# Optimization experiments

Measured on AMD Instinct MI355X. Metric: run time of the kernel, lower is better.

Reference implementation:

```python
import jax, jax.numpy as jnp
import numpy as np

B, SQ, SK, D, H, DFF, L = 8, 1024, 1024, 512, 8, 2048, 2
HD = D // H  # head dim = 64
EPS = 1e-5


def _ln(x, g, b):
    mu = jnp.mean(x, axis=-1, keepdims=True)
    var = jnp.mean((x - mu) ** 2, axis=-1, keepdims=True)
    return (x - mu) * jax.lax.rsqrt(var + EPS) * g + b


def setup_inputs() -> dict:
    key = jax.random.key(0)
    ks = jax.random.split(key, 16)
    std = 0.02
    inp = {
        'q': jax.random.normal(ks[0], (B, SQ, D), jnp.float32),
        'k': jax.random.normal(ks[1], (B, SK, D), jnp.float32),
        'v': jax.random.normal(ks[2], (B, SK, D), jnp.float32),
        # per-layer stacked params (weights stored [in, out])
        'WQ': jax.random.normal(ks[3], (L, D, D), jnp.float32) * std,
        'bQ': jnp.zeros((L, D), jnp.float32),
        'WK': jax.random.normal(ks[4], (L, D, D), jnp.float32) * std,
        'bK': jnp.zeros((L, D), jnp.float32),
        'WV': jax.random.normal(ks[5], (L, D, D), jnp.float32) * std,
        'bV': jnp.zeros((L, D), jnp.float32),
        'WO': jax.random.normal(ks[6], (L, D, D), jnp.float32) * std,
        'bO': jnp.zeros((L, D), jnp.float32),
        'Wf1': jax.random.normal(ks[7], (L, D, DFF), jnp.float32) * std,
        'bf1': jnp.zeros((L, DFF), jnp.float32),
        'Wf2': jax.random.normal(ks[8], (L, DFF, D), jnp.float32) * std,
        'bf2': jnp.zeros((L, D), jnp.float32),
        'ln1_g': jnp.ones((L, D), jnp.float32),
        'ln1_b': jnp.zeros((L, D), jnp.float32),
        'ln2_g': jnp.ones((L, D), jnp.float32),
        'ln2_b': jnp.zeros((L, D), jnp.float32),
        'scale': jnp.full((L,), HD ** -0.5, jnp.float32),       # self.scale init
        'extra_scale': jnp.ones((L,), jnp.float32),             # self.extra_scale init
        'gate_attn': jnp.ones((L,), jnp.float32),
        'gate_ffn': jnp.ones((L,), jnp.float32),
    }
    return inp


def reference(q, k, v, WQ, bQ, WK, bK, WV, bV, WO, bO, Wf1, bf1, Wf2, bf2,
              ln1_g, ln1_b, ln2_g, ln2_b, scale, extra_scale, gate_attn, gate_ffn):
    prev = None  # Realformer residual attention scores
    for i in range(L):
        # QKV projections -> [B, H, S, HD]
        qh = (jnp.einsum('bsd,de->bse', q, WQ[i]) + bQ[i]).reshape(B, SQ, H, HD).transpose(0, 2, 1, 3)
        kh = (jnp.einsum('bsd,de->bse', k, WK[i]) + bK[i]).reshape(B, SK, H, HD).transpose(0, 2, 1, 3)
        vh = (jnp.einsum('bsd,de->bse', v, WV[i]) + bV[i]).reshape(B, SK, H, HD).transpose(0, 2, 1, 3)
        eff_scale = scale[i] * jnp.clip(extra_scale[i], 0.01, 50.0)
        scores = jnp.einsum('bhqd,bhkd->bhqk', qh, kh) * eff_scale  # [B,H,SQ,SK]
        if prev is not None:
            scores = scores + prev
        attn = jax.nn.softmax(scores, axis=-1)
        out = jnp.einsum('bhqk,bhkd->bhqd', attn, vh)
        out = out.transpose(0, 2, 1, 3).reshape(B, SQ, D)
        out = jnp.einsum('bsd,de->bse', out, WO[i]) + bO[i]
        # gated residual + post-norm
        q = q + jax.nn.softplus(gate_attn[i]) * out
        q = _ln(q, ln1_g[i], ln1_b[i])
        # FFN (exact gelu like torch default)
        ff = jax.nn.gelu(jnp.einsum('bsd,df->bsf', q, Wf1[i]) + bf1[i], approximate=False)
        ff = jnp.einsum('bsf,fd->bsd', ff, Wf2[i]) + bf2[i]
        q = q + jax.nn.softplus(gate_ffn[i]) * ff
        q = _ln(q, ln2_g[i], ln2_b[i])
        prev = scores
    return q
```

## Files before the change

### kernel.cpp

```cpp
#include <hip/hip_runtime.h>

#define B_   8
#define SQ_  1024
#define SK_  1024
#define D_   512
#define H_   8
#define DFF_ 2048
#define L_   2
#define HD_  64
#define M_   8192

typedef __bf16 bf16;
using bf16x8 = __attribute__((ext_vector_type(8))) __bf16;
using f32x4  = __attribute__((ext_vector_type(4))) float;

__device__ inline f32x4 mfma16(bf16x8 a, bf16x8 b, f32x4 c) {
  return __builtin_amdgcn_mfma_f32_16x16x32_bf16(a, b, c, 0, 0, 0);
}

__device__ __forceinline__ void gl2lds16(const bf16* g, bf16* l) {
  __builtin_amdgcn_global_load_lds(
      (const __attribute__((address_space(1))) void*)g,
      (__attribute__((address_space(3))) void*)l, 16, 0, 0);
}

__device__ __forceinline__ float gelu_fast(float x) {
  float u = 1.5957691216f * (x + 0.044715f * x * x * x);
  return x / (1.0f + __expf(-u));
}

struct TP4 { const float* in[4]; bf16* out[4]; };
__global__ __launch_bounds__(256) void transpose4_k(TP4 p) {
  __shared__ bf16 tile[32][33];
  int z = blockIdx.z, wsel = z >> 1, l = z & 1;
  const float* inp  = p.in[wsel]  + (size_t)l * D_ * D_;
  bf16*        outp = p.out[wsel] + (size_t)l * D_ * D_;
  int c0 = blockIdx.x * 32, r0 = blockIdx.y * 32;
  int tx = threadIdx.x & 31, ty = threadIdx.x >> 5;
#pragma unroll
  for (int i = 0; i < 32; i += 8)
    tile[ty + i][tx] = (bf16)inp[(size_t)(r0 + ty + i) * D_ + c0 + tx];
  __syncthreads();
#pragma unroll
  for (int i = 0; i < 32; i += 8)
    outp[(size_t)(c0 + ty + i) * D_ + r0 + tx] = tile[tx][ty + i];
}

__global__ __launch_bounds__(256) void transpose_k(
    const float* __restrict__ in, bf16* __restrict__ out, int R, int C) {
  __shared__ bf16 tile[32][33];
  const float* inp  = in  + (size_t)blockIdx.z * R * C;
  bf16*        outp = out + (size_t)blockIdx.z * R * C;
  int c0 = blockIdx.x * 32, r0 = blockIdx.y * 32;
  int tx = threadIdx.x & 31, ty = threadIdx.x >> 5;
#pragma unroll
  for (int i = 0; i < 32; i += 8)
    tile[ty + i][tx] = (bf16)inp[(size_t)(r0 + ty + i) * C + c0 + tx];
  __syncthreads();
#pragma unroll
  for (int i = 0; i < 32; i += 8)
    outp[(size_t)(c0 + ty + i) * R + r0 + tx] = tile[tx][ty + i];
}

__global__ __launch_bounds__(256) void f2b3_k(
    const float* __restrict__ a, const float* __restrict__ b,
    const float* __restrict__ c, bf16* __restrict__ oa,
    bf16* __restrict__ ob, bf16* __restrict__ oc) {
  int which = blockIdx.y;
  const float* in = (which == 0) ? a : (which == 1) ? b : c;
  bf16* out = (which == 0) ? oa : (which == 1) ? ob : oc;
  int i = (blockIdx.x * 256 + threadIdx.x) * 4;
  float4 v = *(const float4*)&in[i];
  out[i] = (bf16)v.x; out[i + 1] = (bf16)v.y;
  out[i + 2] = (bf16)v.z; out[i + 3] = (bf16)v.w;
}

template<int BN>
__global__ __launch_bounds__(256) void gemm_t(
    const bf16* __restrict__ A, const bf16* __restrict__ Bt,
    const float* __restrict__ bias, bf16* __restrict__ Cb,
    float* __restrict__ Cf, int Nsz, int Ksz, int gelu) {
  constexpr int NI = BN / 32;
  __shared__ bf16 As[2][128 * 32];
  __shared__ bf16 Bs[2][BN * 32];
  const int tid = threadIdx.x;
  const int m0 = blockIdx.x * 128, n0 = blockIdx.y * BN;
  const int w = tid >> 6, lane = tid & 63, quad = lane >> 4, l16 = lane & 15;
  const int wm = (w & 1) << 6, wn = (w >> 1) * (BN / 2);
  const int r4 = lane >> 2;
  const int k8 = (lane & 3) * 8;
  f32x4 acc[4][NI] = {};

  auto stage = [&](int k0, int buf) {
    gl2lds16(&A[(size_t)(m0 + w * 16 + r4) * Ksz + k0 + k8],
             &As[buf][(w * 16) * 32]);
    gl2lds16(&A[(size_t)(m0 + (w + 4) * 16 + r4) * Ksz + k0 + k8],
             &As[buf][((w + 4) * 16) * 32]);
    gl2lds16(&Bt[(size_t)(n0 + w * 16 + r4) * Ksz + k0 + k8],
             &Bs[buf][(w * 16) * 32]);
    if constexpr (BN == 128)
      gl2lds16(&Bt[(size_t)(n0 + (w + 4) * 16 + r4) * Ksz + k0 + k8],
               &Bs[buf][((w + 4) * 16) * 32]);
  };

  stage(0, 0);
  __syncthreads();
  int buf = 0;
  for (int k0 = 0; k0 < Ksz; k0 += 32, buf ^= 1) {
    if (k0 + 32 < Ksz) stage(k0 + 32, buf ^ 1);
    bf16x8 af[4], bfr[NI];
#pragma unroll
    for (int i = 0; i < 4; i++)
      af[i] = *(const bf16x8*)&As[buf][(wm + i * 16 + l16) * 32 + quad * 8];
#pragma unroll
    for (int i = 0; i < NI; i++)
      bfr[i] = *(const bf16x8*)&Bs[buf][(wn + i * 16 + l16) * 32 + quad * 8];
#pragma unroll
    for (int mi = 0; mi < 4; mi++)
#pragma unroll
      for (int ni = 0; ni < NI; ni++)
        acc[mi][ni] = mfma16(af[mi], bfr[ni], acc[mi][ni]);
    __syncthreads();
  }
#pragma unroll
  for (int mi = 0; mi < 4; mi++)
#pragma unroll
    for (int ni = 0; ni < NI; ni++) {
      int col = n0 + wn + ni * 16 + l16;
      float bv = bias[col];
#pragma unroll
      for (int r = 0; r < 4; r++) {
        int row = m0 + wm + mi * 16 + quad * 4 + r;
        float x = acc[mi][ni][r] + bv;
        if (gelu) x = gelu_fast(x);
        size_t idx = (size_t)row * Nsz + col;
        if (Cb) Cb[idx] = (bf16)x;
        if (Cf) Cf[idx] = x;
      }
    }
}

struct G256 { const bf16* A; const bf16* Bt; const float* bias; bf16* C; };

#define MFB(mh) \
  _Pragma("unroll") \
  for (int mi = 0; mi < 4; mi++) { \
    _Pragma("unroll") \
    for (int ni = 0; ni < 4; ni++) \
      acc[(mh) * 4 + mi][ni] = mfma16(a[mi], b[ni], acc[(mh) * 4 + mi][ni]); \
  }

#define PHASE(s, mh, STAGE, VM) \
  { \
    if ((mh) == 0) { \
      a[0] = ldA(s, 0); a[1] = ldA(s, 1); a[2] = ldA(s, 2); a[3] = ldA(s, 3); \
      b[0] = ldB(s, 0); b[1] = ldB(s, 1); b[2] = ldB(s, 2); b[3] = ldB(s, 3); \
    } else { \
      a[0] = ldA(s, 4); a[1] = ldA(s, 5); a[2] = ldA(s, 6); a[3] = ldA(s, 7); \
    } \
    STAGE; \
    VM; \
    __builtin_amdgcn_s_barrier(); \
    asm volatile("s_waitcnt lgkmcnt(0)" ::: "memory"); \
    __builtin_amdgcn_sched_barrier(0); \
    __builtin_amdgcn_s_setprio(1); \
    MFB(mh); \
    __builtin_amdgcn_s_setprio(0); \
    __builtin_amdgcn_s_barrier(); \
  }

__global__ __launch_bounds__(512, 2) void gemm256_k(G256 g0, G256 g1,
                                                    int Nsz, int Ksz,
                                                    int gelu) {
  __shared__ bf16 As[4 * 8192];
  __shared__ bf16 Bs[4 * 8192];
  const G256 g = blockIdx.z ? g1 : g0;
  const int tid = threadIdx.x;
  const int w = tid >> 6, lane = tid & 63;
  const int quad = lane >> 4, l16 = lane & 15;
  const int wm = w >> 2, wn = w & 3;
  const int m0 = blockIdx.x * 256, n0 = blockIdx.y * 256;
  const int NCH = Ksz >> 5;
  const int ITERS = NCH >> 2;

  const int srow = tid >> 2;
  const int ssw = ((tid & 3) ^ (srow & 3) ^ ((srow >> 2) & 3)) << 3;
  const int swr = ((quad ^ (l16 & 3) ^ (l16 >> 2)) << 3);

  auto stageA = [&](int kc, int s) {
    const bf16* gp = g.A + (size_t)(m0 + srow) * Ksz + kc * 32 + ssw;
    gl2lds16(gp, &As[s * 8192 + w * 512]);
    gl2lds16(gp + (size_t)128 * Ksz, &As[s * 8192 + 4096 + w * 512]);
  };
  auto stageB = [&](int kc, int s) {
    const bf16* gp = g.Bt + (size_t)(n0 + srow) * Ksz + kc * 32 + ssw;
    gl2lds16(gp, &Bs[s * 8192 + w * 512]);
    gl2lds16(gp + (size_t)128 * Ksz, &Bs[s * 8192 + 4096 + w * 512]);
  };
  auto ldA = [&](int s, int mi) {
    return *(const bf16x8*)&As[s * 8192 + (wm * 128 + mi * 16 + l16) * 32 + swr];
  };
  auto ldB = [&](int s, int ni) {
    return *(const bf16x8*)&Bs[s * 8192 + (wn * 64 + ni * 16 + l16) * 32 + swr];
  };

  f32x4 acc[8][4] = {};

  stageA(0, 0); stageB(0, 0);
  stageA(1, 1); stageB(1, 1);
  stageA(2, 2); stageB(2, 2);
  asm volatile("s_waitcnt vmcnt(4)" ::: "memory");
  __builtin_amdgcn_s_barrier();

  for (int it = 0; it < ITERS; ++it) {
    const int c = it * 4;
    const bool last = (it + 1 == ITERS);
    bf16x8 a[4], b[4];
    PHASE(0, 0, stageA(c + 3, 3), )
    PHASE(0, 1, stageB(c + 3, 3), )
    PHASE(1, 0, if (!last) stageA(c + 4, 0), )
    PHASE(1, 1, if (!last) stageB(c + 4, 0),
          if (!last) { asm volatile("s_waitcnt vmcnt(4)" ::: "memory"); }
          else { asm volatile("s_waitcnt vmcnt(0)" ::: "memory"); })
    PHASE(2, 0, if (!last) stageA(c + 5, 1), )
    PHASE(2, 1, if (!last) stageB(c + 5, 1), )
    PHASE(3, 0, if (!last) stageA(c + 6, 2), )
    PHASE(3, 1, if (!last) stageB(c + 6, 2),
          asm volatile("s_waitcnt vmcnt(4)" ::: "memory"))
  }

#pragma unroll
  for (int mi = 0; mi < 8; mi++)
#pragma unroll
    for (int ni = 0; ni < 4; ni++) {
      const int col = n0 + wn * 64 + ni * 16 + l16;
      const float bv = g.bias[col];
#pragma unroll
      for (int r = 0; r < 4; r++) {
        const int row = m0 + wm * 128 + mi * 16 + quad * 4 + r;
        float x = acc[mi][ni][r] + bv;
        if (gelu) x = gelu_fast(x);
        g.C[(size_t)row * Nsz + col] = (bf16)x;
      }
    }
}

__global__ __launch_bounds__(256) void vtrans2_k(const bf16* __restrict__ vhh,
                                                 bf16* __restrict__ vt0,
                                                 bf16* __restrict__ vt1) {
  __shared__ bf16 sm[64][72];
  int kt = blockIdx.x, bh = blockIdx.y, z = blockIdx.z;
  int coloff = z ? D_ : 0;
  bf16* vt = z ? vt1 : vt0;
  int b = bh >> 3, h = bh & 7;
  int tid = threadIdx.x;
  for (int c = tid; c < 512; c += 256) {
    int key = c >> 3, off = (c & 7) * 8;
    *(uint4*)&sm[key][off] = *(const uint4*)
        &vhh[(size_t)(b * SK_ + kt * 64 + key) * (2 * D_) + coloff + h * 64 + off];
  }
  __syncthreads();
  for (int c = tid; c < 512; c += 256) {
    int hd = c >> 3, koff = (c & 7) * 8;
    bf16 tmp[8];
#pragma unroll
    for (int j = 0; j < 8; j++) tmp[j] = sm[koff + j][hd];
    *(uint4*)&vt[(size_t)(bh * 64 + hd) * SK_ + kt * 64 + koff] = *(uint4*)tmp;
  }
}

template<bool HAS0>
__global__ __launch_bounds__(256) void attn_t(
    const bf16* __restrict__ qh, const bf16* __restrict__ qh0,
    const bf16* __restrict__ kh, const bf16* __restrict__ kh0, int kstride,
    const bf16* __restrict__ vt, const float* __restrict__ scale,
    const float* __restrict__ extra, int li, bf16* __restrict__ ctx) {
  __shared__ bf16 Ks[2 * 2 * 2048];
  __shared__ bf16 K0s[HAS0 ? 2 * 2 * 2048 : 64];
  __shared__ bf16 Vs[2 * 2 * 2048];
  __shared__ bf16 Ps[4][16 * 72];
  int qt = blockIdx.x, bh = blockIdx.y;
  int b = bh >> 3, h = bh & 7;
  int tid = threadIdx.x, w = tid >> 6, lane = tid & 63;
  int quad = lane >> 4, l16 = lane & 15;
  const int r4 = lane >> 2, c4 = (lane & 3) * 8;
  float eff1 = scale[li] * fminf(fmaxf(extra[li], 0.01f), 50.0f);
  float eff0 = HAS0 ? scale[li - 1] * fminf(fmaxf(extra[li - 1], 0.01f), 50.0f) : 0.f;
  bf16x8 aq[2][2], aq0[2][2];
#pragma unroll
  for (int mi = 0; mi < 2; mi++) {
    int qrow = b * SQ_ + qt * 128 + w * 32 + mi * 16 + l16;
    const bf16* qp = qh + (size_t)qrow * D_ + h * 64 + quad * 8;
    aq[mi][0] = *(const bf16x8*)qp; aq[mi][1] = *(const bf16x8*)(qp + 32);
#pragma unroll
    for (int k2 = 0; k2 < 2; k2++)
#pragma unroll
      for (int j = 0; j < 8; j++)
        aq[mi][k2][j] = (bf16)((float)aq[mi][k2][j] * eff1);
    if constexpr (HAS0) {
      const bf16* qp0 = qh0 + (size_t)qrow * D_ + h * 64 + quad * 8;
      aq0[mi][0] = *(const bf16x8*)qp0; aq0[mi][1] = *(const bf16x8*)(qp0 + 32);
#pragma unroll
      for (int k2 = 0; k2 < 2; k2++)
#pragma unroll
        for (int j = 0; j < 8; j++)
          aq0[mi][k2][j] = (bf16)((float)aq0[mi][k2][j] * eff0);
    }
  }
  bf16x8 ones;
#pragma unroll
  for (int j = 0; j < 8; j++) ones[j] = (bf16)1.0f;

  f32x4 o[2][4] = {};
  f32x4 ol[2] = {};

  auto stage = [&](int kt, int bufi) {
    size_t kg = (size_t)(b * SK_ + kt * 64 + w * 16 + r4) * kstride + h * 64 + c4;
    gl2lds16(&kh[kg],      &Ks[(bufi * 2 + 0) * 2048 + (w * 16) * 32]);
    gl2lds16(&kh[kg + 32], &Ks[(bufi * 2 + 1) * 2048 + (w * 16) * 32]);
    if constexpr (HAS0) {
      gl2lds16(&kh0[kg],      &K0s[(bufi * 2 + 0) * 2048 + (w * 16) * 32]);
      gl2lds16(&kh0[kg + 32], &K0s[(bufi * 2 + 1) * 2048 + (w * 16) * 32]);
    }
    size_t vg = (size_t)(bh * 64 + w * 16 + r4) * SK_ + kt * 64 + c4;
    gl2lds16(&vt[vg],      &Vs[(bufi * 2 + 0) * 2048 + (w * 16) * 32]);
    gl2lds16(&vt[vg + 32], &Vs[(bufi * 2 + 1) * 2048 + (w * 16) * 32]);
  };

  stage(0, 0);
  __syncthreads();
  int buf = 0;
  for (int kt = 0; kt < SK_ / 64; kt++, buf ^= 1) {
    if (kt + 1 < SK_ / 64) stage(kt + 1, buf ^ 1);
    bf16x8 bv[2][4];
#pragma unroll
    for (int kk = 0; kk < 2; kk++)
#pragma unroll
      for (int ni = 0; ni < 4; ni++)
        bv[kk][ni] = *(const bf16x8*)&Vs[kk * 2048 + buf * 4096 +
                                         (ni * 16 + l16) * 32 + quad * 8];
#pragma unroll
    for (int mi = 0; mi < 2; mi++) {
#pragma unroll
      for (int ni = 0; ni < 4; ni++) {
        int ro = (ni * 16 + l16) * 32 + quad * 8;
        f32x4 t = {};
        t = mfma16(aq[mi][0], *(const bf16x8*)&Ks[0 * 2048 + buf * 4096 + ro], t);
        t = mfma16(aq[mi][1], *(const bf16x8*)&Ks[1 * 2048 + buf * 4096 + ro], t);
        if constexpr (HAS0) {
          t = mfma16(aq0[mi][0], *(const bf16x8*)&K0s[0 * 2048 + buf * 4096 + ro], t);
          t = mfma16(aq0[mi][1], *(const bf16x8*)&K0s[1 * 2048 + buf * 4096 + ro], t);
        }
#pragma unroll
        for (int r = 0; r < 4; r++)
          Ps[w][(quad * 4 + r) * 72 + ni * 16 + l16] = (bf16)__expf(t[r]);
      }
#pragma unroll
      for (int kk = 0; kk < 2; kk++) {
        bf16x8 ap = *(const bf16x8*)&Ps[w][l16 * 72 + kk * 32 + quad * 8];
        ol[mi] = mfma16(ap, ones, ol[mi]);
#pragma unroll
        for (int ni = 0; ni < 4; ni++)
          o[mi][ni] = mfma16(ap, bv[kk][ni], o[mi][ni]);
      }
    }
    __syncthreads();
  }
#pragma unroll
  for (int mi = 0; mi < 2; mi++)
#pragma unroll
    for (int ni = 0; ni < 4; ni++)
#pragma unroll
      for (int r = 0; r < 4; r++) {
        int row = b * SQ_ + qt * 128 + w * 32 + mi * 16 + quad * 4 + r;
        ctx[(size_t)row * D_ + h * 64 + ni * 16 + l16] =
            (bf16)(o[mi][ni][r] / ol[mi][r]);
      }
}

__global__ __launch_bounds__(256) void ln_k(
    const float* __restrict__ cur_in, const float* __restrict__ add,
    const float* __restrict__ gate, const float* __restrict__ g,
    const float* __restrict__ bb, float* __restrict__ outf,
    bf16* __restrict__ outb) {
  int row = blockIdx.x, tid = threadIdx.x;
  float gv = gate[0];
  float sp = gv > 20.f ? gv : log1pf(expf(gv));
  size_t base = (size_t)row * D_;
  int c0 = tid * 2;
  float2 c2 = *(const float2*)&cur_in[base + c0];
  float2 a2 = *(const float2*)&add[base + c0];
  float x0 = c2.x + sp * a2.x, x1 = c2.y + sp * a2.y;
  float s = x0 + x1, s2 = x0 * x0 + x1 * x1;
#pragma unroll
  for (int m = 1; m < 64; m <<= 1) {
    s += __shfl_xor(s, m);
    s2 += __shfl_xor(s2, m);
  }
  __shared__ float sa[4], sb[4];
  int w = tid >> 6;
  if ((tid & 63) == 0) { sa[w] = s; sb[w] = s2; }
  __syncthreads();
  s = sa[0] + sa[1] + sa[2] + sa[3];
  s2 = sb[0] + sb[1] + sb[2] + sb[3];
  float mu = s * (1.f / D_);
  float var = s2 * (1.f / D_) - mu * mu;
  float rs = rsqrtf(var + 1e-5f);
  float y0 = (x0 - mu) * rs * g[c0] + bb[c0];
  float y1 = (x1 - mu) * rs * g[c0 + 1] + bb[c0 + 1];
  if (outf) { float2 y; y.x = y0; y.y = y1; *(float2*)&outf[base + c0] = y; }
  if (outb) { outb[base + c0] = (bf16)y0; outb[base + c0 + 1] = (bf16)y1; }
}

extern "C" void kernel_launch(void* const* d_in, const int* in_sizes, int n_in,
                              void* d_out, int out_size, void* d_ws,
                              size_t ws_size, hipStream_t stream) {
  const float* qin = (const float*)d_in[0];
  const float* kin = (const float*)d_in[1];
  const float* vin = (const float*)d_in[2];
  const float* WQ  = (const float*)d_in[3];
  const float* bQ  = (const float*)d_in[4];
  const float* WK  = (const float*)d_in[5];
  const float* bK  = (const float*)d_in[6];
  const float* WV  = (const float*)d_in[7];
  const float* bV  = (const float*)d_in[8];
  const float* WO  = (const float*)d_in[9];
  const float* bO  = (const float*)d_in[10];
  const float* Wf1 = (const float*)d_in[11];
  const float* bf1 = (const float*)d_in[12];
  const float* Wf2 = (const float*)d_in[13];
  const float* bf2 = (const float*)d_in[14];
  const float* l1g = (const float*)d_in[15];
  const float* l1b = (const float*)d_in[16];
  const float* l2g = (const float*)d_in[17];
  const float* l2b = (const float*)d_in[18];
  const float* sc  = (const float*)d_in[19];
  const float* ex  = (const float*)d_in[20];
  const float* ga  = (const float*)d_in[21];
  const float* gf  = (const float*)d_in[22];

  char* p = (char*)d_ws;
  auto alloc = [&](size_t bytes) {
    void* r = (void*)p;
    p += (bytes + 255) & ~(size_t)255;
    return r;
  };
  bf16* WQt  = (bf16*)alloc((size_t)L_ * D_ * D_ * 2);
  bf16* WKt  = (bf16*)alloc((size_t)L_ * D_ * D_ * 2);
  bf16* WVt  = (bf16*)alloc((size_t)L_ * D_ * D_ * 2);
  bf16* WOt  = (bf16*)alloc((size_t)L_ * D_ * D_ * 2);
  bf16* Wf1t = (bf16*)alloc((size_t)L_ * D_ * DFF_ * 2);
  bf16* Wf2t = (bf16*)alloc((size_t)L_ * D_ * DFF_ * 2);
  float* cur  = (float*)alloc((size_t)M_ * D_ * 4);
  bf16* curb  = (bf16*)alloc((size_t)M_ * D_ * 2);
  bf16* qb    = (bf16*)alloc((size_t)M_ * D_ * 2);
  bf16* kb    = (bf16*)alloc((size_t)M_ * D_ * 2);
  bf16* vb    = (bf16*)alloc((size_t)M_ * D_ * 2);
  bf16* khh   = (bf16*)alloc((size_t)M_ * 2 * D_ * 2);
  bf16* vhh   = (bf16*)alloc((size_t)M_ * 2 * D_ * 2);
  bf16* qh0b  = (bf16*)alloc((size_t)M_ * D_ * 2);
  bf16* qh1b  = (bf16*)alloc((size_t)M_ * D_ * 2);
  bf16* vt0   = (bf16*)alloc((size_t)M_ * D_ * 2);
  bf16* vt1   = (bf16*)alloc((size_t)M_ * D_ * 2);
  bf16* ctx   = (bf16*)alloc((size_t)M_ * D_ * 2);
  float* proj = (float*)alloc((size_t)M_ * D_ * 4);
  bf16* ffmid = (bf16*)alloc((size_t)M_ * DFF_ * 2);
  float* ffout = (float*)alloc((size_t)M_ * D_ * 4);

  TP4 tp; tp.in[0] = WQ; tp.in[1] = WK; tp.in[2] = WV; tp.in[3] = WO;
  tp.out[0] = WQt; tp.out[1] = WKt; tp.out[2] = WVt; tp.out[3] = WOt;
  transpose4_k<<<dim3(16, 16, 8), 256, 0, stream>>>(tp);
  transpose_k<<<dim3(DFF_ / 32, D_ / 32, L_), 256, 0, stream>>>(Wf1, Wf1t, D_, DFF_);
  transpose_k<<<dim3(D_ / 32, DFF_ / 32, L_), 256, 0, stream>>>(Wf2, Wf2t, DFF_, D_);
  f2b3_k<<<dim3((M_ * D_) / 1024, 3), 256, 0, stream>>>(qin, kin, vin, qb, kb, vb);

  G256 gk; gk.A = kb; gk.Bt = WKt; gk.bias = bK; gk.C = khh;
  G256 gvv; gvv.A = vb; gvv.Bt = WVt; gvv.bias = bV; gvv.C = vhh;
  gemm256_k<<<dim3(M_ / 256, (2 * D_) / 256, 2), 512, 0, stream>>>(
      gk, gvv, 2 * D_, D_, 0);
  vtrans2_k<<<dim3(SK_ / 64, B_ * H_, 2), 256, 0, stream>>>(vhh, vt0, vt1);
  gemm_t<64><<<dim3(M_ / 128, 8), 256, 0, stream>>>(
      qb, WQt, bQ, qh0b, nullptr, D_, D_, 0);

  for (int li = 0; li < L_; li++) {
    if (li > 0)
      gemm_t<64><<<dim3(M_ / 128, 8), 256, 0, stream>>>(
          curb, WQt + (size_t)li * D_ * D_, bQ + li * D_, qh1b, nullptr, D_, D_, 0);
    if (li == 0)
      attn_t<false><<<dim3(SQ_ / 128, B_ * H_), 256, 0, stream>>>(
          qh0b, qh0b, khh, khh, 2 * D_, vt0, sc, ex, 0, ctx);
    else
      attn_t<true><<<dim3(SQ_ / 128, B_ * H_), 256, 0, stream>>>(
          qh1b, qh0b, khh + (size_t)li * D_, khh, 2 * D_, vt1, sc, ex, 1, ctx);
    gemm_t<64><<<dim3(M_ / 128, 8), 256, 0, stream>>>(
        ctx, WOt + (size_t)li * D_ * D_, bO + li * D_, nullptr, proj, D_, D_, 0);
    ln_k<<<M_, 256, 0, stream>>>((li == 0) ? qin : cur, proj, ga + li,
                                 l1g + li * D_, l1b + li * D_, cur, curb);
    G256 gf1; gf1.A = curb; gf1.Bt = Wf1t + (size_t)li * D_ * DFF_;
    gf1.bias = bf1 + li * DFF_; gf1.C = ffmid;
    gemm256_k<<<dim3(M_ / 256, DFF_ / 256, 1), 512, 0, stream>>>(
        gf1, gf1, DFF_, D_, 1);
    gemm_t<64><<<dim3(M_ / 128, 8), 256, 0, stream>>>(
        ffmid, Wf2t + (size_t)li * DFF_ * D_, bf2 + li * D_, nullptr, ffout,
        D_, DFF_, 0);
    ln_k<<<M_, 256, 0, stream>>>(cur, ffout, gf + li, l2g + li * D_,
                                 l2b + li * D_,
                                 (li == L_ - 1) ? (float*)d_out : cur,
                                 (li == L_ - 1) ? nullptr : curb);
  }
}
```

Baseline: 527.4 us.

## Replace N=512 GEMMs with 128x128 tile, 4-stage pipelined swizzled kernel

Replaces the 128x64 double-buffered gemm_t with a new 512-thread gemm128_k using 128x128 tiles, a 4-deep global-to-LDS pipeline with explicit vmcnt waits, an XOR-swizzled LDS layout, and setprio around MFMA bursts. It is used for the Q, O, FFN2 and layer-1 Q projections. Larger tiles raise data reuse, deeper prefetch hides load latency, and the swizzle reduces LDS bank conflicts. The grid shrinks from 512 to 256 blocks, which may underfill the GPU, and the per-wave MFMA work per barrier is small.

```diff
diff --git a/kernel.cpp b/kernel.cpp
--- a/kernel.cpp
+++ b/kernel.cpp
@@ -73,71 +73,6 @@
   float4 v = *(const float4*)&in[i];
   out[i] = (bf16)v.x; out[i + 1] = (bf16)v.y;
   out[i + 2] = (bf16)v.z; out[i + 3] = (bf16)v.w;
-}
-
-template<int BN>
-__global__ __launch_bounds__(256) void gemm_t(
-    const bf16* __restrict__ A, const bf16* __restrict__ Bt,
-    const float* __restrict__ bias, bf16* __restrict__ Cb,
-    float* __restrict__ Cf, int Nsz, int Ksz, int gelu) {
-  constexpr int NI = BN / 32;
-  __shared__ bf16 As[2][128 * 32];
-  __shared__ bf16 Bs[2][BN * 32];
-  const int tid = threadIdx.x;
-  const int m0 = blockIdx.x * 128, n0 = blockIdx.y * BN;
-  const int w = tid >> 6, lane = tid & 63, quad = lane >> 4, l16 = lane & 15;
-  const int wm = (w & 1) << 6, wn = (w >> 1) * (BN / 2);
-  const int r4 = lane >> 2;
-  const int k8 = (lane & 3) * 8;
-  f32x4 acc[4][NI] = {};
-
-  auto stage = [&](int k0, int buf) {
-    gl2lds16(&A[(size_t)(m0 + w * 16 + r4) * Ksz + k0 + k8],
-             &As[buf][(w * 16) * 32]);
-    gl2lds16(&A[(size_t)(m0 + (w + 4) * 16 + r4) * Ksz + k0 + k8],
-             &As[buf][((w + 4) * 16) * 32]);
-    gl2lds16(&Bt[(size_t)(n0 + w * 16 + r4) * Ksz + k0 + k8],
-             &Bs[buf][(w * 16) * 32]);
-    if constexpr (BN == 128)
-      gl2lds16(&Bt[(size_t)(n0 + (w + 4) * 16 + r4) * Ksz + k0 + k8],
-               &Bs[buf][((w + 4) * 16) * 32]);
-  };
-
-  stage(0, 0);
-  __syncthreads();
-  int buf = 0;
-  for (int k0 = 0; k0 < Ksz; k0 += 32, buf ^= 1) {
-    if (k0 + 32 < Ksz) stage(k0 + 32, buf ^ 1);
-    bf16x8 af[4], bfr[NI];
-#pragma unroll
-    for (int i = 0; i < 4; i++)
-      af[i] = *(const bf16x8*)&As[buf][(wm + i * 16 + l16) * 32 + quad * 8];
-#pragma unroll
-    for (int i = 0; i < NI; i++)
-      bfr[i] = *(const bf16x8*)&Bs[buf][(wn + i * 16 + l16) * 32 + quad * 8];
-#pragma unroll
-    for (int mi = 0; mi < 4; mi++)
-#pragma unroll
-      for (int ni = 0; ni < NI; ni++)
-        acc[mi][ni] = mfma16(af[mi], bfr[ni], acc[mi][ni]);
-    __syncthreads();
-  }
-#pragma unroll
-  for (int mi = 0; mi < 4; mi++)
-#pragma unroll
-    for (int ni = 0; ni < NI; ni++) {
-      int col = n0 + wn + ni * 16 + l16;
-      float bv = bias[col];
-#pragma unroll
-      for (int r = 0; r < 4; r++) {
-        int row = m0 + wm + mi * 16 + quad * 4 + r;
-        float x = acc[mi][ni][r] + bv;
-        if (gelu) x = gelu_fast(x);
-        size_t idx = (size_t)row * Nsz + col;
-        if (Cb) Cb[idx] = (bf16)x;
-        if (Cf) Cf[idx] = x;
-      }
-    }
 }
 
 struct G256 { const bf16* A; const bf16* Bt; const float* bias; bf16* C; };
@@ -241,6 +176,89 @@
         float x = acc[mi][ni][r] + bv;
         if (gelu) x = gelu_fast(x);
         g.C[(size_t)row * Nsz + col] = (bf16)x;
+      }
+    }
+}
+
+__global__ __launch_bounds__(512, 2) void gemm128_k(
+    const bf16* __restrict__ A, const bf16* __restrict__ Bt,
+    const float* __restrict__ bias, bf16* __restrict__ Cb,
+    float* __restrict__ Cf, int Nsz, int Ksz) {
+  __shared__ bf16 As[4 * 4096];
+  __shared__ bf16 Bs[4 * 4096];
+  const int tid = threadIdx.x;
+  const int w = tid >> 6, lane = tid & 63;
+  const int quad = lane >> 4, l16 = lane & 15;
+  const int wm = w >> 2, wn = w & 3;
+  const int m0 = blockIdx.x * 128, n0 = blockIdx.y * 128;
+  const int NCH = Ksz >> 5;
+
+  const int srow = tid >> 2;
+  const int ssw = ((tid & 3) ^ (srow & 3) ^ ((srow >> 2) & 3)) << 3;
+  const int swr = ((quad ^ (l16 & 3) ^ (l16 >> 2)) << 3);
+
+  auto stageChunk = [&](int kc) {
+    const int s = kc & 3;
+    gl2lds16(A + (size_t)(m0 + srow) * Ksz + kc * 32 + ssw,
+             &As[s * 4096 + w * 512]);
+    gl2lds16(Bt + (size_t)(n0 + srow) * Ksz + kc * 32 + ssw,
+             &Bs[s * 4096 + w * 512]);
+  };
+  auto ldA = [&](int s, int mi) {
+    return *(const bf16x8*)&As[s * 4096 + (wm * 64 + mi * 16 + l16) * 32 + swr];
+  };
+  auto ldB = [&](int s, int ni) {
+    return *(const bf16x8*)&Bs[s * 4096 + (wn * 32 + ni * 16 + l16) * 32 + swr];
+  };
+
+  f32x4 acc[4][2] = {};
+
+  stageChunk(0); stageChunk(1); stageChunk(2);
+  asm volatile("s_waitcnt vmcnt(4)" ::: "memory");
+  __builtin_amdgcn_s_barrier();
+
+  auto phase = [&](int c, int vml) {
+    const int s = c & 3;
+    if (vml == 4) stageChunk(c + 3);
+    bf16x8 a0 = ldA(s, 0), a1 = ldA(s, 1), a2 = ldA(s, 2), a3 = ldA(s, 3);
+    bf16x8 b0 = ldB(s, 0), b1 = ldB(s, 1);
+    if (vml == 4)      asm volatile("s_waitcnt vmcnt(4)" ::: "memory");
+    else if (vml == 2) asm volatile("s_waitcnt vmcnt(2)" ::: "memory");
+    else if (vml == 0) asm volatile("s_waitcnt vmcnt(0)" ::: "memory");
+    __builtin_amdgcn_s_barrier();
+    asm volatile("s_waitcnt lgkmcnt(0)" ::: "memory");
+    __builtin_amdgcn_sched_barrier(0);
+    __builtin_amdgcn_s_setprio(1);
+    acc[0][0] = mfma16(a0, b0, acc[0][0]);
+    acc[0][1] = mfma16(a0, b1, acc[0][1]);
+    acc[1][0] = mfma16(a1, b0, acc[1][0]);
+    acc[1][1] = mfma16(a1, b1, acc[1][1]);
+    acc[2][0] = mfma16(a2, b0, acc[2][0]);
+    acc[2][1] = mfma16(a2, b1, acc[2][1]);
+    acc[3][0] = mfma16(a3, b0, acc[3][0]);
+    acc[3][1] = mfma16(a3, b1, acc[3][1]);
+    __builtin_amdgcn_s_setprio(0);
+    __builtin_amdgcn_s_barrier();
+  };
+
+  for (int c = 0; c + 4 <= NCH; ++c) phase(c, 4);
+  phase(NCH - 3, 2);
+  phase(NCH - 2, 0);
+  phase(NCH - 1, -1);
+
+#pragma unroll
+  for (int mi = 0; mi < 4; mi++)
+#pragma unroll
+    for (int ni = 0; ni < 2; ni++) {
+      const int col = n0 + wn * 32 + ni * 16 + l16;
+      const float bv = bias[col];
+#pragma unroll
+      for (int r = 0; r < 4; r++) {
+        const int row = m0 + wm * 64 + mi * 16 + quad * 4 + r;
+        float x = acc[mi][ni][r] + bv;
+        size_t idx = (size_t)row * Nsz + col;
+        if (Cb) Cb[idx] = (bf16)x;
+        if (Cf) Cf[idx] = x;
       }
     }
 }
@@ -479,30 +497,30 @@
   gemm256_k<<<dim3(M_ / 256, (2 * D_) / 256, 2), 512, 0, stream>>>(
       gk, gvv, 2 * D_, D_, 0);
   vtrans2_k<<<dim3(SK_ / 64, B_ * H_, 2), 256, 0, stream>>>(vhh, vt0, vt1);
-  gemm_t<64><<<dim3(M_ / 128, 8), 256, 0, stream>>>(
-      qb, WQt, bQ, qh0b, nullptr, D_, D_, 0);
+  gemm128_k<<<dim3(M_ / 128, 4), 512, 0, stream>>>(
+      qb, WQt, bQ, qh0b, nullptr, D_, D_);
 
   for (int li = 0; li < L_; li++) {
     if (li > 0)
-      gemm_t<64><<<dim3(M_ / 128, 8), 256, 0, stream>>>(
-          curb, WQt + (size_t)li * D_ * D_, bQ + li * D_, qh1b, nullptr, D_, D_, 0);
+      gemm128_k<<<dim3(M_ / 128, 4), 512, 0, stream>>>(
+          curb, WQt + (size_t)li * D_ * D_, bQ + li * D_, qh1b, nullptr, D_, D_);
     if (li == 0)
       attn_t<false><<<dim3(SQ_ / 128, B_ * H_), 256, 0, stream>>>(
           qh0b, qh0b, khh, khh, 2 * D_, vt0, sc, ex, 0, ctx);
     else
       attn_t<true><<<dim3(SQ_ / 128, B_ * H_), 256, 0, stream>>>(
           qh1b, qh0b, khh + (size_t)li * D_, khh, 2 * D_, vt1, sc, ex, 1, ctx);
-    gemm_t<64><<<dim3(M_ / 128, 8), 256, 0, stream>>>(
-        ctx, WOt + (size_t)li * D_ * D_, bO + li * D_, nullptr, proj, D_, D_, 0);
+    gemm128_k<<<dim3(M_ / 128, 4), 512, 0, stream>>>(
+        ctx, WOt + (size_t)li * D_ * D_, bO + li * D_, nullptr, proj, D_, D_);
     ln_k<<<M_, 256, 0, stream>>>((li == 0) ? qin : cur, proj, ga + li,
                                  l1g + li * D_, l1b + li * D_, cur, curb);
     G256 gf1; gf1.A = curb; gf1.Bt = Wf1t + (size_t)li * D_ * DFF_;
     gf1.bias = bf1 + li * DFF_; gf1.C = ffmid;
     gemm256_k<<<dim3(M_ / 256, DFF_ / 256, 1), 512, 0, stream>>>(
         gf1, gf1, DFF_, D_, 1);
-    gemm_t<64><<<dim3(M_ / 128, 8), 256, 0, stream>>>(
+    gemm128_k<<<dim3(M_ / 128, 4), 512, 0, stream>>>(
         ffmid, Wf2t + (size_t)li * DFF_ * D_, bf2 + li * D_, nullptr, ffout,
-        D_, DFF_, 0);
+        D_, DFF_);
     ln_k<<<M_, 256, 0, stream>>>(cur, ffout, gf + li, l2g + li * D_,
                                  l2b + li * D_,
                                  (li == L_ - 1) ? (float*)d_out : cur,
```

Result: no change. 534.9 us (+1.4%).
